# Kernel optimization log

Hardware: AMD Instinct MI355X
Metric: run time of the kernel (lower is better)

The kernel has to match this reference:

```python
import jax, jax.numpy as jnp
import numpy as np

N = 50000
E = 800000
IN_DIM = 512
HID = 64
OUT = 64
HEADS = 4
NEG_SLOPE = 0.2


def setup_inputs() -> dict:
    key = jax.random.key(0)
    ks = jax.random.split(key, 16)
    s = 0.05
    inp = {
        "x": jax.random.normal(ks[0], (N, IN_DIM), jnp.float32),
        "edge_index": jax.random.randint(ks[1], (2, E), 0, N, jnp.int64),
        # layer 1: in=512 -> heads*hid = 4*64 = 256, concat=True
        "W1l": jax.random.normal(ks[2], (IN_DIM, HEADS * HID), jnp.float32) * s,
        "b1l": jnp.zeros((HEADS * HID,), jnp.float32),
        "W1r": jax.random.normal(ks[3], (IN_DIM, HEADS * HID), jnp.float32) * s,
        "b1r": jnp.zeros((HEADS * HID,), jnp.float32),
        "att1": jax.random.normal(ks[4], (HEADS, HID), jnp.float32) * s,
        "bias1": jnp.zeros((HEADS * HID,), jnp.float32),
        # layer 2: in=256 -> heads*(2*out) = 4*128, concat=False (mean heads)
        "W2l": jax.random.normal(ks[5], (HEADS * HID, HEADS * 2 * OUT), jnp.float32) * s,
        "b2l": jnp.zeros((HEADS * 2 * OUT,), jnp.float32),
        "W2r": jax.random.normal(ks[6], (HEADS * HID, HEADS * 2 * OUT), jnp.float32) * s,
        "b2r": jnp.zeros((HEADS * 2 * OUT,), jnp.float32),
        "att2": jax.random.normal(ks[7], (HEADS, 2 * OUT), jnp.float32) * s,
        "bias2": jnp.zeros((2 * OUT,), jnp.float32),
    }
    return inp


def _gatv2(x, src, dst, Wl, bl, Wr, br, att, bias, concat):
    """GATv2Conv (PyG semantics): message x_l[src], attention over incoming edges per dst."""
    H, C = att.shape
    n = x.shape[0]
    xl = (x @ Wl + bl).reshape(n, H, C)  # source transform (messages)
    xr = (x @ Wr + br).reshape(n, H, C)  # target transform
    g = jax.nn.leaky_relu(xl[src] + xr[dst], NEG_SLOPE)   # [E, H, C]
    e = jnp.einsum('ehc,hc->eh', g, att)                  # [E, H]
    # numerically-stable softmax over irregular neighbor sets (segmented by dst)
    m = jax.ops.segment_max(e, dst, num_segments=n)
    ex = jnp.exp(e - m[dst])
    denom = jax.ops.segment_sum(ex, dst, num_segments=n)
    alpha = ex / (denom[dst] + 1e-16)                     # [E, H]
    out = jax.ops.segment_sum(xl[src] * alpha[..., None], dst, num_segments=n)  # [N, H, C]
    if concat:
        return out.reshape(n, H * C) + bias
    return out.mean(axis=1) + bias


def reference(x, edge_index, W1l, b1l, W1r, b1r, att1, bias1,
              W2l, b2l, W2r, b2r, att2, bias2):
    # add self loops (PyG add_self_loops=True default)
    loops = jnp.arange(N, dtype=edge_index.dtype)
    src = jnp.concatenate([edge_index[0], loops])
    dst = jnp.concatenate([edge_index[1], loops])
    h = jax.nn.relu(_gatv2(x, src, dst, W1l, b1l, W1r, b1r, att1, bias1, concat=True))
    return _gatv2(h, src, dst, W2l, b2l, W2r, b2r, att2, bias2, concat=False)
```

## Files before the change

### kernel.cpp

```cpp
#include <hip/hip_runtime.h>

#define NNODES 50000
#define NEDGES 800000
#define ET (NEDGES + NNODES)
#define HEADS 4

typedef __attribute__((ext_vector_type(8))) short bf16x8;
typedef __attribute__((ext_vector_type(4))) float f32x4;

#define EXP2F(x) __builtin_amdgcn_exp2f(x)

#define GLOAD16(g, l) __builtin_amdgcn_global_load_lds(                      \
    (const __attribute__((address_space(1))) unsigned int*)(g),              \
    (__attribute__((address_space(3))) unsigned int*)(l), 16, 0, 0)

__device__ inline unsigned short f2bf(float f) {
  union { float f; unsigned int i; } c; c.f = f;
  unsigned int b = c.i + 0x7fffu + ((c.i >> 16) & 1u);
  return (unsigned short)(b >> 16);
}
__device__ inline float4 b4tof(uint2 r) {
  float4 f;
  union { unsigned int i; float v; } c;
  c.i = r.x << 16;          f.x = c.v;
  c.i = r.x & 0xffff0000u;  f.y = c.v;
  c.i = r.y << 16;          f.z = c.v;
  c.i = r.y & 0xffff0000u;  f.w = c.v;
  return f;
}


__global__ void k_hist(const int* __restrict__ ei, int* __restrict__ deg) {
  int i = blockIdx.x * blockDim.x + threadIdx.x;
  if (i >= ET) return;
  int dst = (i < NEDGES) ? ei[NEDGES + i] : (i - NEDGES);
  atomicAdd(&deg[dst], 1);
}

__global__ void k_scan1(const int* __restrict__ deg, int* __restrict__ part,
                        int* __restrict__ bsum, int n) {
  __shared__ int s[256];
  int tid = threadIdx.x;
  int i = blockIdx.x * 256 + tid;
  int v = (i < n) ? deg[i] : 0;
  s[tid] = v;
  __syncthreads();
  for (int off = 1; off < 256; off <<= 1) {
    int t = (tid >= off) ? s[tid - off] : 0;
    __syncthreads();
    s[tid] += t;
    __syncthreads();
  }
  if (i < n) part[i] = s[tid] - v;
  if (tid == 255) bsum[blockIdx.x] = s[255];
}

__global__ void k_scan2(int* bsum, int nb) {
  __shared__ int s[256];
  int t = threadIdx.x;
  int v = (t < nb) ? bsum[t] : 0;
  s[t] = v;
  __syncthreads();
  for (int off = 1; off < 256; off <<= 1) {
    int tv = (t >= off) ? s[t - off] : 0;
    __syncthreads();
    s[t] += tv;
    __syncthreads();
  }
  if (t < nb) bsum[t] = s[t] - v;
}

__global__ void k_scan3(const int* __restrict__ part, const int* __restrict__ bsum,
                        int* __restrict__ rowstart, int* __restrict__ cursor,
                        int n, int total) {
  int i = blockIdx.x * blockDim.x + threadIdx.x;
  if (i < n) {
    int v = part[i] + bsum[i >> 8];
    rowstart[i] = v;
    cursor[i] = v;
  }
  if (i == n) rowstart[n] = total;
}

__global__ void k_scatter(const int* __restrict__ ei, int* __restrict__ cursor,
                          int* __restrict__ csrsrc) {
  int i = blockIdx.x * blockDim.x + threadIdx.x;
  if (i >= ET) return;
  int src, dst;
  if (i < NEDGES) { src = ei[i]; dst = ei[NEDGES + i]; }
  else            { src = dst = i - NEDGES; }
  int pos = atomicAdd(&cursor[dst], 1);
  csrsrc[pos] = src;
}


__global__ void k_cast_bf16(const float* __restrict__ in, unsigned short* __restrict__ out, int n4) {
  int i = blockIdx.x * blockDim.x + threadIdx.x;
  if (i >= n4) return;
  float4 v = ((const float4*)in)[i];
  ushort4 o;
  o.x = f2bf(v.x); o.y = f2bf(v.y); o.z = f2bf(v.z); o.w = f2bf(v.w);
  ((ushort4*)out)[i] = o;
}

__global__ __launch_bounds__(256) void k_castw_all(
    const float* __restrict__ W1l, const float* __restrict__ W1r,
    const float* __restrict__ W2l, const float* __restrict__ W2r,
    unsigned short* __restrict__ w1t, unsigned short* __restrict__ w2t) {
  __shared__ float tile[32][33];
  int which = blockIdx.y;
  const float* W;
  unsigned short* T;
  int K, N, noff;
  if (which == 0)      { W = W1l; T = w1t; K = 512; N = 256; noff = 0; }
  else if (which == 1) { W = W1r; T = w1t; K = 512; N = 256; noff = 256; }
  else if (which == 2) { W = W2l; T = w2t; K = 256; N = 512; noff = 0; }
  else                 { W = W2r; T = w2t; K = 256; N = 512; noff = 512; }
  int tpr = N >> 5;
  int tk = (blockIdx.x / tpr) << 5;
  int tn = (blockIdx.x % tpr) << 5;
  int c = threadIdx.x & 31, r = threadIdx.x >> 5;
#pragma unroll
  for (int rr = 0; rr < 32; rr += 8)
    tile[r + rr][c] = W[(size_t)(tk + r + rr) * N + tn + c];
  __syncthreads();
#pragma unroll
  for (int rr = 0; rr < 32; rr += 8)
    T[(size_t)(tn + r + rr + noff) * K + tk + c] = f2bf(tile[c][r + rr]);
}


__global__ __launch_bounds__(256) void k_gemm(
    const unsigned short* __restrict__ A, const unsigned short* __restrict__ Bt,
    const float* __restrict__ bL, const float* __restrict__ bR, int nsplit,
    unsigned short* __restrict__ C, int M, int K, int N) {
  __shared__ unsigned short As[2][128 * 32];
  __shared__ unsigned short Bs[2][128 * 32];
  int tid = threadIdx.x;
  int lane = tid & 63, wave = tid >> 6;
  int wr = (wave >> 1) * 64, wc = (wave & 1) * 64;
  int row0 = blockIdx.x * 128, col0 = blockIdx.y * 128;
  int fr = lane & 15, fq = lane >> 4;
  int sr = tid >> 2, sc = (tid & 3) * 8;

  const unsigned short* ga0 = &A[(size_t)(row0 + sr) * K + sc];
  const unsigned short* ga1 = &A[(size_t)(row0 + sr + 64) * K + sc];
  const unsigned short* gb0 = &Bt[(size_t)(col0 + sr) * K + sc];
  const unsigned short* gb1 = &Bt[(size_t)(col0 + sr + 64) * K + sc];

  f32x4 acc[4][4] = {};
  const int NT = K >> 5;

  GLOAD16(ga0, &As[0][tid * 8]);
  GLOAD16(ga1, &As[0][2048 + tid * 8]);
  GLOAD16(gb0, &Bs[0][tid * 8]);
  GLOAD16(gb1, &Bs[0][2048 + tid * 8]);
  asm volatile("s_waitcnt vmcnt(0)" ::: "memory");
  __builtin_amdgcn_s_barrier();

  int cur = 0;
  for (int t = 0; t < NT; ++t) {
    if (t + 1 < NT) {
      int k0 = (t + 1) << 5;
      GLOAD16(ga0 + k0, &As[cur ^ 1][tid * 8]);
      GLOAD16(ga1 + k0, &As[cur ^ 1][2048 + tid * 8]);
      GLOAD16(gb0 + k0, &Bs[cur ^ 1][tid * 8]);
      GLOAD16(gb1 + k0, &Bs[cur ^ 1][2048 + tid * 8]);
    }
    bf16x8 af[4], bfr[4];
#pragma unroll
    for (int m = 0; m < 4; ++m)
      af[m] = *(const bf16x8*)&As[cur][(wr + m * 16 + fr) * 32 + fq * 8];
#pragma unroll
    for (int n = 0; n < 4; ++n)
      bfr[n] = *(const bf16x8*)&Bs[cur][(wc + n * 16 + fr) * 32 + fq * 8];
#pragma unroll
    for (int m = 0; m < 4; ++m)
#pragma unroll
      for (int n = 0; n < 4; ++n)
        acc[m][n] = __builtin_amdgcn_mfma_f32_16x16x32_bf16(af[m], bfr[n], acc[m][n], 0, 0, 0);
    asm volatile("s_waitcnt vmcnt(0)" ::: "memory");
    __builtin_amdgcn_s_barrier();
    cur ^= 1;
  }

#pragma unroll
  for (int m = 0; m < 4; ++m) {
#pragma unroll
    for (int n = 0; n < 4; ++n) {
      int col = col0 + wc + n * 16 + fr;
      float bv = (col < nsplit) ? bL[col] : bR[col - nsplit];
#pragma unroll
      for (int j = 0; j < 4; ++j) {
        int row = row0 + wr + m * 16 + fq * 4 + j;
        if (row < M) C[(size_t)row * N + col] = f2bf(acc[m][n][j] + bv);
      }
    }
  }
}


template <int CQ>
__device__ inline void load_row(const unsigned short* p, float4* xv) {
  if constexpr (CQ == 1) {
    xv[0] = b4tof(*(const uint2*)p);
  } else {
    uint4 r = *(const uint4*)p;
    xv[0] = b4tof(make_uint2(r.x, r.y));
    xv[1] = b4tof(make_uint2(r.z, r.w));
  }
}

template <int CQ>
__device__ inline float edge_score(const float4* xv, const float4* xrv, const float4* attv) {
  float p = 0.f;
#pragma unroll
  for (int q = 0; q < CQ; ++q) {
    float s;
    s = xv[q].x + xrv[q].x; p = fmaf(attv[q].x, fmaxf(s, 0.2f * s), p);
    s = xv[q].y + xrv[q].y; p = fmaf(attv[q].y, fmaxf(s, 0.2f * s), p);
    s = xv[q].z + xrv[q].z; p = fmaf(attv[q].z, fmaxf(s, 0.2f * s), p);
    s = xv[q].w + xrv[q].w; p = fmaf(attv[q].w, fmaxf(s, 0.2f * s), p);
  }
  return p;
}

template <int CQ, int MODE, int STR>
__global__ __launch_bounds__(256) void k_fused(
    const int* __restrict__ rowstart, const int* __restrict__ csrsrc,
    const unsigned short* __restrict__ xlr,
    const float* __restrict__ att, const float* __restrict__ bias,
    void* __restrict__ outp) {
  const int C = CQ * 64;
  const int CHL = CQ * 4;
  int dst = (blockIdx.x * blockDim.x + threadIdx.x) >> 6;
  int lane = threadIdx.x & 63;
  if (dst >= NNODES) return;
  int h = lane >> 4;
  int l = lane & 15;
  const int choff = h * C + l * CHL;

  float4 xrv[CQ], attv[CQ];
  load_row<CQ>(&xlr[(size_t)dst * STR + STR / 2 + choff], xrv);
#pragma unroll
  for (int q = 0; q < CQ; ++q) {
    float4 a = *(const float4*)&att[choff + q * 4];
    a.x *= 1.44269504f; a.y *= 1.44269504f;
    a.z *= 1.44269504f; a.w *= 1.44269504f;
    attv[q] = a;
  }

  int rs = __builtin_amdgcn_readfirstlane(rowstart[dst]);
  int re = __builtin_amdgcn_readfirstlane(rowstart[dst + 1]);

  float den = 0.f;
  float4 acc[CQ];
#pragma unroll
  for (int q = 0; q < CQ; ++q) acc[q] = make_float4(0.f, 0.f, 0.f, 0.f);

  int i = rs;
  for (; i + 4 <= re; i += 4) {
    int s0 = csrsrc[i + 0];
    int s1 = csrsrc[i + 1];
    int s2 = csrsrc[i + 2];
    int s3 = csrsrc[i + 3];
    float4 x0[CQ], x1[CQ], x2[CQ], x3[CQ];
    load_row<CQ>(&xlr[(unsigned)s0 * (unsigned)STR + choff], x0);
    load_row<CQ>(&xlr[(unsigned)s1 * (unsigned)STR + choff], x1);
    load_row<CQ>(&xlr[(unsigned)s2 * (unsigned)STR + choff], x2);
    load_row<CQ>(&xlr[(unsigned)s3 * (unsigned)STR + choff], x3);
    float p0 = edge_score<CQ>(x0, xrv, attv);
    float p1 = edge_score<CQ>(x1, xrv, attv);
    float p2 = edge_score<CQ>(x2, xrv, attv);
    float p3 = edge_score<CQ>(x3, xrv, attv);
#pragma unroll
    for (int d = 1; d <= 8; d <<= 1) {
      p0 += __shfl_xor(p0, d);
      p1 += __shfl_xor(p1, d);
      p2 += __shfl_xor(p2, d);
      p3 += __shfl_xor(p3, d);
    }
    float w0 = EXP2F(p0), w1 = EXP2F(p1), w2 = EXP2F(p2), w3 = EXP2F(p3);
    den += (w0 + w1) + (w2 + w3);
#pragma unroll
    for (int q = 0; q < CQ; ++q) {
      acc[q].x = fmaf(w0, x0[q].x, fmaf(w1, x1[q].x, fmaf(w2, x2[q].x, fmaf(w3, x3[q].x, acc[q].x))));
      acc[q].y = fmaf(w0, x0[q].y, fmaf(w1, x1[q].y, fmaf(w2, x2[q].y, fmaf(w3, x3[q].y, acc[q].y))));
      acc[q].z = fmaf(w0, x0[q].z, fmaf(w1, x1[q].z, fmaf(w2, x2[q].z, fmaf(w3, x3[q].z, acc[q].z))));
      acc[q].w = fmaf(w0, x0[q].w, fmaf(w1, x1[q].w, fmaf(w2, x2[q].w, fmaf(w3, x3[q].w, acc[q].w))));
    }
  }
  for (; i < re; ++i) {
    int s0 = csrsrc[i];
    float4 x0[CQ];
    load_row<CQ>(&xlr[(unsigned)s0 * (unsigned)STR + choff], x0);
    float p0 = edge_score<CQ>(x0, xrv, attv);
#pragma unroll
    for (int d = 1; d <= 8; d <<= 1) p0 += __shfl_xor(p0, d);
    float w0 = EXP2F(p0);
    den += w0;
#pragma unroll
    for (int q = 0; q < CQ; ++q) {
      acc[q].x = fmaf(w0, x0[q].x, acc[q].x);
      acc[q].y = fmaf(w0, x0[q].y, acc[q].y);
      acc[q].z = fmaf(w0, x0[q].z, acc[q].z);
      acc[q].w = fmaf(w0, x0[q].w, acc[q].w);
    }
  }

  float inv = 1.f / (den + 1e-16f);

  if (MODE == 0) {
    unsigned short* out = (unsigned short*)outp;
#pragma unroll
    for (int q = 0; q < CQ; ++q) {
      const float4 bv = *(const float4*)&bias[choff + q * 4];
      ushort4 o;
      o.x = f2bf(fmaxf(acc[q].x * inv + bv.x, 0.f));
      o.y = f2bf(fmaxf(acc[q].y * inv + bv.y, 0.f));
      o.z = f2bf(fmaxf(acc[q].z * inv + bv.z, 0.f));
      o.w = f2bf(fmaxf(acc[q].w * inv + bv.w, 0.f));
      *(ushort4*)&out[(size_t)dst * (HEADS * C) + choff + q * 4] = o;
    }
  } else {
    float* out = (float*)outp;
    float r[CQ][4];
#pragma unroll
    for (int q = 0; q < CQ; ++q) {
      r[q][0] = acc[q].x * inv; r[q][1] = acc[q].y * inv;
      r[q][2] = acc[q].z * inv; r[q][3] = acc[q].w * inv;
    }
#pragma unroll
    for (int q = 0; q < CQ; ++q)
#pragma unroll
      for (int j = 0; j < 4; ++j) {
        r[q][j] += __shfl_xor(r[q][j], 16);
        r[q][j] += __shfl_xor(r[q][j], 32);
      }
    if (lane < 16) {
#pragma unroll
      for (int q = 0; q < CQ; ++q) {
        int c = lane * CHL + q * 4;
        float4 o;
        o.x = r[q][0] * 0.25f + bias[c + 0];
        o.y = r[q][1] * 0.25f + bias[c + 1];
        o.z = r[q][2] * 0.25f + bias[c + 2];
        o.w = r[q][3] * 0.25f + bias[c + 3];
        *(float4*)&out[(size_t)dst * C + c] = o;
      }
    }
  }
}


extern "C" void kernel_launch(void* const* d_in, const int* in_sizes, int n_in,
                              void* d_out, int out_size, void* d_ws, size_t ws_size,
                              hipStream_t stream) {
  (void)in_sizes; (void)n_in; (void)out_size; (void)ws_size;
  const float* x     = (const float*)d_in[0];
  const int*   ei    = (const int*)d_in[1];
  const float* W1l   = (const float*)d_in[2];
  const float* b1l   = (const float*)d_in[3];
  const float* W1r   = (const float*)d_in[4];
  const float* b1r   = (const float*)d_in[5];
  const float* att1  = (const float*)d_in[6];
  const float* bias1 = (const float*)d_in[7];
  const float* W2l   = (const float*)d_in[8];
  const float* b2l   = (const float*)d_in[9];
  const float* W2r   = (const float*)d_in[10];
  const float* b2r   = (const float*)d_in[11];
  const float* att2  = (const float*)d_in[12];
  const float* bias2 = (const float*)d_in[13];
  float* out = (float*)d_out;

  char* ws = (char*)d_ws;
  size_t off = 0;
  auto alloc = [&](size_t bytes) {
    char* p = ws + off;
    off = (off + bytes + 255) & ~(size_t)255;
    return p;
  };
  int*  deg      = (int*)alloc((size_t)NNODES * 4);
  int*  part     = (int*)alloc((size_t)NNODES * 4);
  int*  bsum     = (int*)alloc(256 * 4);
  int*  rowstart = (int*)alloc((size_t)(NNODES + 1) * 4);
  int*  cursor   = (int*)alloc((size_t)NNODES * 4);
  int*  csrsrc   = (int*)alloc((size_t)ET * 4);
  unsigned short* xb   = (unsigned short*)alloc((size_t)NNODES * 512 * 2);
  unsigned short* w1t  = (unsigned short*)alloc((size_t)512 * 512 * 2);
  unsigned short* w2t  = (unsigned short*)alloc((size_t)1024 * 256 * 2);
  unsigned short* xlr1 = (unsigned short*)alloc((size_t)NNODES * 512 * 2);
  unsigned short* hbuf = (unsigned short*)alloc((size_t)NNODES * 256 * 2);
  unsigned short* xlr2 = (unsigned short*)alloc((size_t)NNODES * 1024 * 2);
  (void)alloc(64 * 1024);

  (void)hipMemsetAsync(deg, 0, (size_t)NNODES * 4, stream);
  k_hist<<<(ET + 255) / 256, 256, 0, stream>>>(ei, deg);
  int nb = (NNODES + 255) / 256;
  k_scan1<<<nb, 256, 0, stream>>>(deg, part, bsum, NNODES);
  k_scan2<<<1, 256, 0, stream>>>(bsum, nb);
  k_scan3<<<(NNODES + 256) / 256, 256, 0, stream>>>(part, bsum, rowstart, cursor, NNODES, ET);
  k_scatter<<<(ET + 255) / 256, 256, 0, stream>>>(ei, cursor, csrsrc);

  k_cast_bf16<<<(NNODES * 512 / 4 + 255) / 256, 256, 0, stream>>>(x, xb, NNODES * 512 / 4);
  k_castw_all<<<dim3(128, 4), 256, 0, stream>>>(W1l, W1r, W2l, W2r, w1t, w2t);

  const int gridM = (NNODES + 127) / 128;
  const int gridFused = (NNODES + 3) / 4;

  k_gemm<<<dim3(gridM, 4), 256, 0, stream>>>(xb, w1t, b1l, b1r, 256, xlr1, NNODES, 512, 512);
  k_fused<1, 0, 512><<<gridFused, 256, 0, stream>>>(rowstart, csrsrc, xlr1, att1, bias1, hbuf);

  k_gemm<<<dim3(gridM, 8), 256, 0, stream>>>(hbuf, w2t, b2l, b2r, 512, xlr2, NNODES, 256, 1024);
  k_fused<2, 1, 1024><<<gridFused, 256, 0, stream>>>(rowstart, csrsrc, xlr2, att2, bias2, out);
}
```

Measured before the change: 468.1 us.

## Triple-buffer GEMM LDS loads and rewrite leaky-ReLU score as abs-fma

The bf16 MFMA GEMM goes from double to triple buffering of its LDS tiles. Partial vmcnt waits keep two future tiles in flight while the current one is computed, with an explicit lgkmcnt wait and barrier before each buffer is reused. Separately, the edge-score leaky-ReLU is rewritten as 0.4*(1.5*s+|s|), with the 0.4 folded into the pre-scaled attention vector, so each element needs one fma plus an abs instead of a mul plus a max. The triple buffer uses more LDS, which can lower occupancy, and the pipeline assumes NT>=3, which holds for K=256 and K=512.

```diff
diff --git a/kernel.cpp b/kernel.cpp
--- a/kernel.cpp
+++ b/kernel.cpp
@@ -130,12 +130,18 @@
 }
 
 
+template <int N> __device__ __forceinline__ void waitvm() {
+  if constexpr (N == 0) asm volatile("s_waitcnt vmcnt(0)" ::: "memory");
+  else if constexpr (N == 4) asm volatile("s_waitcnt vmcnt(4)" ::: "memory");
+  else asm volatile("s_waitcnt vmcnt(8)" ::: "memory");
+}
+
 __global__ __launch_bounds__(256) void k_gemm(
     const unsigned short* __restrict__ A, const unsigned short* __restrict__ Bt,
     const float* __restrict__ bL, const float* __restrict__ bR, int nsplit,
     unsigned short* __restrict__ C, int M, int K, int N) {
-  __shared__ unsigned short As[2][128 * 32];
-  __shared__ unsigned short Bs[2][128 * 32];
+  __shared__ unsigned short As[3][128 * 32];
+  __shared__ unsigned short Bs[3][128 * 32];
   int tid = threadIdx.x;
   int lane = tid & 63, wave = tid >> 6;
   int wr = (wave >> 1) * 64, wc = (wave & 1) * 64;
@@ -151,38 +157,50 @@
   f32x4 acc[4][4] = {};
   const int NT = K >> 5;
 
-  GLOAD16(ga0, &As[0][tid * 8]);
-  GLOAD16(ga1, &As[0][2048 + tid * 8]);
-  GLOAD16(gb0, &Bs[0][tid * 8]);
-  GLOAD16(gb1, &Bs[0][2048 + tid * 8]);
-  asm volatile("s_waitcnt vmcnt(0)" ::: "memory");
-  __builtin_amdgcn_s_barrier();
-
-  int cur = 0;
-  for (int t = 0; t < NT; ++t) {
-    if (t + 1 < NT) {
-      int k0 = (t + 1) << 5;
-      GLOAD16(ga0 + k0, &As[cur ^ 1][tid * 8]);
-      GLOAD16(ga1 + k0, &As[cur ^ 1][2048 + tid * 8]);
-      GLOAD16(gb0 + k0, &Bs[cur ^ 1][tid * 8]);
-      GLOAD16(gb1 + k0, &Bs[cur ^ 1][2048 + tid * 8]);
-    }
-    bf16x8 af[4], bfr[4];
-#pragma unroll
-    for (int m = 0; m < 4; ++m)
-      af[m] = *(const bf16x8*)&As[cur][(wr + m * 16 + fr) * 32 + fq * 8];
-#pragma unroll
-    for (int n = 0; n < 4; ++n)
-      bfr[n] = *(const bf16x8*)&Bs[cur][(wc + n * 16 + fr) * 32 + fq * 8];
-#pragma unroll
-    for (int m = 0; m < 4; ++m)
-#pragma unroll
-      for (int n = 0; n < 4; ++n)
-        acc[m][n] = __builtin_amdgcn_mfma_f32_16x16x32_bf16(af[m], bfr[n], acc[m][n], 0, 0, 0);
-    asm volatile("s_waitcnt vmcnt(0)" ::: "memory");
+#define STAGE(b, k0)                                  \
+  do {                                                \
+    GLOAD16(ga0 + (k0), &As[b][tid * 8]);             \
+    GLOAD16(ga1 + (k0), &As[b][2048 + tid * 8]);      \
+    GLOAD16(gb0 + (k0), &Bs[b][tid * 8]);             \
+    GLOAD16(gb1 + (k0), &Bs[b][2048 + tid * 8]);      \
+  } while (0)
+
+#define COMPUTE(b)                                                        \
+  do {                                                                    \
+    bf16x8 af[4], bfr[4];                                                 \
+    _Pragma("unroll")                                                     \
+    for (int m = 0; m < 4; ++m)                                           \
+      af[m] = *(const bf16x8*)&As[b][(wr + m * 16 + fr) * 32 + fq * 8];   \
+    _Pragma("unroll")                                                     \
+    for (int n = 0; n < 4; ++n)                                           \
+      bfr[n] = *(const bf16x8*)&Bs[b][(wc + n * 16 + fr) * 32 + fq * 8];  \
+    _Pragma("unroll")                                                     \
+    for (int m = 0; m < 4; ++m)                                           \
+      _Pragma("unroll")                                                   \
+      for (int n = 0; n < 4; ++n)                                         \
+        acc[m][n] = __builtin_amdgcn_mfma_f32_16x16x32_bf16(af[m], bfr[n], acc[m][n], 0, 0, 0); \
+  } while (0)
+
+  STAGE(0, 0);
+  STAGE(1, 32);
+  STAGE(2, 64);
+
+  for (int t = 0; t < NT - 3; ++t) {
+    int b = t % 3;
+    waitvm<8>();
     __builtin_amdgcn_s_barrier();
-    cur ^= 1;
-  }
+    COMPUTE(b);
+    asm volatile("s_waitcnt lgkmcnt(0)" ::: "memory");
+    __builtin_amdgcn_sched_barrier(0);
+    __builtin_amdgcn_s_barrier();
+    STAGE(b, (t + 3) << 5);
+  }
+  waitvm<8>(); __builtin_amdgcn_s_barrier(); COMPUTE((NT - 3) % 3);
+  waitvm<4>(); __builtin_amdgcn_s_barrier(); COMPUTE((NT - 2) % 3);
+  waitvm<0>(); __builtin_amdgcn_s_barrier(); COMPUTE((NT - 1) % 3);
+
+#undef STAGE
+#undef COMPUTE
 
 #pragma unroll
   for (int m = 0; m < 4; ++m) {
@@ -212,15 +230,15 @@
 }
 
 template <int CQ>
-__device__ inline float edge_score(const float4* xv, const float4* xrv, const float4* attv) {
+__device__ inline float edge_score(const float4* xv, const float4* xrv, const float4* a04) {
   float p = 0.f;
 #pragma unroll
   for (int q = 0; q < CQ; ++q) {
     float s;
-    s = xv[q].x + xrv[q].x; p = fmaf(attv[q].x, fmaxf(s, 0.2f * s), p);
-    s = xv[q].y + xrv[q].y; p = fmaf(attv[q].y, fmaxf(s, 0.2f * s), p);
-    s = xv[q].z + xrv[q].z; p = fmaf(attv[q].z, fmaxf(s, 0.2f * s), p);
-    s = xv[q].w + xrv[q].w; p = fmaf(attv[q].w, fmaxf(s, 0.2f * s), p);
+    s = xv[q].x + xrv[q].x; p = fmaf(a04[q].x, fmaf(1.5f, s, fabsf(s)), p);
+    s = xv[q].y + xrv[q].y; p = fmaf(a04[q].y, fmaf(1.5f, s, fabsf(s)), p);
+    s = xv[q].z + xrv[q].z; p = fmaf(a04[q].z, fmaf(1.5f, s, fabsf(s)), p);
+    s = xv[q].w + xrv[q].w; p = fmaf(a04[q].w, fmaf(1.5f, s, fabsf(s)), p);
   }
   return p;
 }
@@ -240,14 +258,14 @@
   int l = lane & 15;
   const int choff = h * C + l * CHL;
 
-  float4 xrv[CQ], attv[CQ];
+  float4 xrv[CQ], a04[CQ];
   load_row<CQ>(&xlr[(size_t)dst * STR + STR / 2 + choff], xrv);
 #pragma unroll
   for (int q = 0; q < CQ; ++q) {
     float4 a = *(const float4*)&att[choff + q * 4];
-    a.x *= 1.44269504f; a.y *= 1.44269504f;
-    a.z *= 1.44269504f; a.w *= 1.44269504f;
-    attv[q] = a;
+    const float k = 0.4f * 1.44269504f;
+    a.x *= k; a.y *= k; a.z *= k; a.w *= k;
+    a04[q] = a;
   }
 
   int rs = __builtin_amdgcn_readfirstlane(rowstart[dst]);
@@ -269,10 +287,10 @@
     load_row<CQ>(&xlr[(unsigned)s1 * (unsigned)STR + choff], x1);
     load_row<CQ>(&xlr[(unsigned)s2 * (unsigned)STR + choff], x2);
     load_row<CQ>(&xlr[(unsigned)s3 * (unsigned)STR + choff], x3);
-    float p0 = edge_score<CQ>(x0, xrv, attv);
-    float p1 = edge_score<CQ>(x1, xrv, attv);
-    float p2 = edge_score<CQ>(x2, xrv, attv);
-    float p3 = edge_score<CQ>(x3, xrv, attv);
+    float p0 = edge_score<CQ>(x0, xrv, a04);
+    float p1 = edge_score<CQ>(x1, xrv, a04);
+    float p2 = edge_score<CQ>(x2, xrv, a04);
+    float p3 = edge_score<CQ>(x3, xrv, a04);
 #pragma unroll
     for (int d = 1; d <= 8; d <<= 1) {
       p0 += __shfl_xor(p0, d);
@@ -294,7 +312,7 @@
     int s0 = csrsrc[i];
     float4 x0[CQ];
     load_row<CQ>(&xlr[(unsigned)s0 * (unsigned)STR + choff], x0);
-    float p0 = edge_score<CQ>(x0, xrv, attv);
+    float p0 = edge_score<CQ>(x0, xrv, a04);
 #pragma unroll
     for (int d = 1; d <= 8; d <<= 1) p0 += __shfl_xor(p0, d);
     float w0 = EXP2F(p0);
```

Measured after the change: 453.6 us. -3.1%, faster.
